# Performance work log

Measured on AMD Instinct MI355X. Metric: run time of the kernel, lower is better.

Reference implementation:

```python
import jax, jax.numpy as jnp
import numpy as np

COST_CLASS, COST_BBOX, COST_GIOU = 1.0, 5.0, 2.0
NUM_CLASSES = 80
BS, T, Q = 16, 32, 1024


def box_cxcywh_to_xyxy(b):
    cx, cy, w, h = jnp.split(b, 4, axis=-1)
    return jnp.concatenate([cx - 0.5 * w, cy - 0.5 * h, cx + 0.5 * w, cy + 0.5 * h], axis=-1)


def generalized_box_iou(b1, b2):
    # b1: [..., Q, 4] xyxy, b2: [..., 1, 4] xyxy -> [..., Q]
    area1 = (b1[..., 2] - b1[..., 0]) * (b1[..., 3] - b1[..., 1])
    area2 = (b2[..., 2] - b2[..., 0]) * (b2[..., 3] - b2[..., 1])
    lt = jnp.maximum(b1[..., :2], b2[..., :2])
    rb = jnp.minimum(b1[..., 2:], b2[..., 2:])
    wh = jnp.clip(rb - lt, 0.0)
    inter = wh[..., 0] * wh[..., 1]
    union = area1 + area2 - inter
    iou = inter / union
    lt_c = jnp.minimum(b1[..., :2], b2[..., :2])
    rb_c = jnp.maximum(b1[..., 2:], b2[..., 2:])
    wh_c = jnp.clip(rb_c - lt_c, 0.0)
    area_c = wh_c[..., 0] * wh_c[..., 1]
    return iou - (area_c - union) / area_c


def setup_inputs() -> dict:
    key = jax.random.key(0)
    k1, k2, k3, k4, k5 = jax.random.split(key, 5)
    return {
        "pred_logits": jax.random.normal(k1, (BS, T, Q, NUM_CLASSES), dtype=jnp.float32),
        "pred_logits_b": jax.random.normal(k2, (BS, T, Q, 2), dtype=jnp.float32),
        "pred_boxes": jax.random.uniform(k3, (BS, T, Q, 4), dtype=jnp.float32),
        "tgt_bbox": jax.random.uniform(k4, (BS, T, 1, 4), dtype=jnp.float32),
        "tgt_ids": jax.random.randint(k5, (BS * T,), 0, NUM_CLASSES, dtype=jnp.int64),
    }


def reference(pred_logits, pred_logits_b, pred_boxes, tgt_bbox, tgt_ids):
    bs, t, q = pred_logits.shape[0], pred_logits.shape[1], pred_logits.shape[2]
    # L1 cdist between each prediction and the single target box per frame: [bs,t,Q,1]
    cost_bbox = jnp.sum(jnp.abs(pred_boxes - tgt_bbox), axis=-1, keepdims=True)
    # GIoU cost: [bs,t,Q,1]
    cost_giou = -generalized_box_iou(
        box_cxcywh_to_xyxy(pred_boxes), box_cxcywh_to_xyxy(tgt_bbox)
    )[..., None]
    # binary objectness cost: -P(object): [bs,t,Q,1]
    cost_class = -jax.nn.softmax(pred_logits_b, axis=-1)[..., 1:2]
    C = COST_BBOX * cost_bbox + COST_CLASS * cost_class + COST_GIOU * cost_giou
    # Hungarian assignment on a Qx1 cost matrix == argmin over queries per frame
    rows = jnp.argmin(C[..., 0], axis=-1).reshape(bs * t)  # [bs*t] selected query idx
    # majority vote over all frames (the module returns the mode as the final idx)
    mode_idx = jnp.argmax(jnp.bincount(rows, length=q))
    return C, rows, mode_idx


if __name__ == "__main__":
    out = reference(**setup_inputs())
    print(out[0].shape, out[1].shape, out[2])
```

## Files before the change

kernel.cpp:

```cpp
#include <hip/hip_runtime.h>

#define NFRAMES 512
#define NQ      1024
#define CSIZE   (NFRAMES * NQ)

__global__ __launch_bounds__(256) void cost_argmin_kernel(
    const float* __restrict__ logits_b,
    const float* __restrict__ boxes,
    const float* __restrict__ tgt,
    float* __restrict__ out)
{
#pragma clang fp contract(off)
    const int f   = blockIdx.x;
    const int tid = threadIdx.x;

    const float4 tb = *reinterpret_cast<const float4*>(tgt + (size_t)f * 4);
    const float tx0 = tb.x - 0.5f * tb.z, ty0 = tb.y - 0.5f * tb.w;
    const float tx1 = tb.x + 0.5f * tb.z, ty1 = tb.y + 0.5f * tb.w;
    const float area2 = (tx1 - tx0) * (ty1 - ty0);

    const float* fb = boxes    + (size_t)f * NQ * 4;
    const float* fl = logits_b + (size_t)f * NQ * 2;
    float*       fc = out      + (size_t)f * NQ;

    float bestv = INFINITY;
    int   besti = 0;

    #pragma unroll
    for (int k = 0; k < 4; ++k) {
        const int q = tid + k * 256;
        const float4 pb = *reinterpret_cast<const float4*>(fb + q * 4);
        const float2 lg = *reinterpret_cast<const float2*>(fl + q * 2);

        const float cb = fabsf(pb.x - tb.x) + fabsf(pb.y - tb.y)
                       + fabsf(pb.z - tb.z) + fabsf(pb.w - tb.w);

        const float px0 = pb.x - 0.5f * pb.z, py0 = pb.y - 0.5f * pb.w;
        const float px1 = pb.x + 0.5f * pb.z, py1 = pb.y + 0.5f * pb.w;
        const float area1 = (px1 - px0) * (py1 - py0);

        const float ltx = fmaxf(px0, tx0), lty = fmaxf(py0, ty0);
        const float rbx = fminf(px1, tx1), rby = fminf(py1, ty1);
        const float whx = fmaxf(rbx - ltx, 0.0f), why = fmaxf(rby - lty, 0.0f);
        const float inter = whx * why;
        const float uni   = area1 + area2 - inter;
        const float iou   = inter / uni;

        const float lcx = fminf(px0, tx0), lcy = fminf(py0, ty0);
        const float rcx = fmaxf(px1, tx1), rcy = fmaxf(py1, ty1);
        const float wcx = fmaxf(rcx - lcx, 0.0f), wcy = fmaxf(rcy - lcy, 0.0f);
        const float areac = wcx * wcy;
        const float giou  = iou - (areac - uni) / areac;
        const float cg    = -giou;

        const float m  = fmaxf(lg.x, lg.y);
        const float e0 = expf(lg.x - m), e1 = expf(lg.y - m);
        const float cc = -(e1 / (e0 + e1));

        const float c = 5.0f * cb + 1.0f * cc + 2.0f * cg;
        fc[q] = c;

        if (c < bestv) { bestv = c; besti = q; }
    }

    __shared__ float sv[256];
    __shared__ int   si[256];
    sv[tid] = bestv; si[tid] = besti;
    __syncthreads();
    for (int s = 128; s > 0; s >>= 1) {
        if (tid < s) {
            const float v2 = sv[tid + s];
            const int   i2 = si[tid + s];
            if (v2 < sv[tid] || (v2 == sv[tid] && i2 < si[tid])) { sv[tid] = v2; si[tid] = i2; }
        }
        __syncthreads();
    }
    if (tid == 0) out[CSIZE + f] = (float)si[0];
}

__global__ __launch_bounds__(1024) void mode_kernel(float* __restrict__ out)
{
    __shared__ int counts[NQ];
    __shared__ int sc[NQ];
    __shared__ int si[NQ];
    const int tid = threadIdx.x;

    counts[tid] = 0;
    __syncthreads();
    if (tid < NFRAMES) {
        const int r = (int)out[CSIZE + tid];
        atomicAdd(&counts[r], 1);
    }
    __syncthreads();

    sc[tid] = counts[tid];
    si[tid] = tid;
    __syncthreads();
    for (int s = 512; s > 0; s >>= 1) {
        if (tid < s) {
            const int c2 = sc[tid + s];
            const int i2 = si[tid + s];
            if (c2 > sc[tid] || (c2 == sc[tid] && i2 < si[tid])) { sc[tid] = c2; si[tid] = i2; }
        }
        __syncthreads();
    }
    if (tid == 0) out[CSIZE + NFRAMES] = (float)si[0];
}

extern "C" void kernel_launch(void* const* d_in, const int* in_sizes, int n_in,
                              void* d_out, int out_size, void* d_ws, size_t ws_size,
                              hipStream_t stream) {
    const float* logits_b = (const float*)d_in[1];
    const float* boxes    = (const float*)d_in[2];
    const float* tgt      = (const float*)d_in[3];
    float* out = (float*)d_out;

    hipLaunchKernelGGL(cost_argmin_kernel, dim3(NFRAMES), dim3(256), 0, stream,
                       logits_b, boxes, tgt, out);
    hipLaunchKernelGGL(mode_kernel, dim3(1), dim3(1024), 0, stream, out);
}
```

Before: 210.0 us.

## Fuse mode computation into cost kernel via global histogram and last-block reduction

Removes the separate single-block mode kernel. Each block atomically adds its argmin row to a global histogram, and the last block to finish (found through an atomic counter) reduces the histogram to pick the mode. This saves one kernel launch and its serial dependency. In exchange it adds a hipMemsetAsync of the workspace on every call and global atomics with a thread fence.

```diff
diff --git a/kernel.cpp b/kernel.cpp
--- a/kernel.cpp
+++ b/kernel.cpp
@@ -4,15 +4,22 @@
 #define NQ      1024
 #define CSIZE   (NFRAMES * NQ)
 
-__global__ __launch_bounds__(256) void cost_argmin_kernel(
+__global__ __launch_bounds__(256) void fused_matcher_kernel(
     const float* __restrict__ logits_b,
     const float* __restrict__ boxes,
     const float* __restrict__ tgt,
-    float* __restrict__ out)
+    float* __restrict__ out,
+    int* __restrict__ bins,
+    int* __restrict__ counter)
 {
 #pragma clang fp contract(off)
     const int f   = blockIdx.x;
     const int tid = threadIdx.x;
+
+    __shared__ float sv[256];
+    __shared__ int   si[256];
+    __shared__ int   scc[256];
+    __shared__ int   is_last;
 
     const float4 tb = *reinterpret_cast<const float4*>(tgt + (size_t)f * 4);
     const float tx0 = tb.x - 0.5f * tb.z, ty0 = tb.y - 0.5f * tb.w;
@@ -63,8 +70,6 @@
         if (c < bestv) { bestv = c; besti = q; }
     }
 
-    __shared__ float sv[256];
-    __shared__ int   si[256];
     sv[tid] = bestv; si[tid] = besti;
     __syncthreads();
     for (int s = 128; s > 0; s >>= 1) {
@@ -75,36 +80,41 @@
         }
         __syncthreads();
     }
-    if (tid == 0) out[CSIZE + f] = (float)si[0];
-}
 
-__global__ __launch_bounds__(1024) void mode_kernel(float* __restrict__ out)
-{
-    __shared__ int counts[NQ];
-    __shared__ int sc[NQ];
-    __shared__ int si[NQ];
-    const int tid = threadIdx.x;
-
-    counts[tid] = 0;
-    __syncthreads();
-    if (tid < NFRAMES) {
-        const int r = (int)out[CSIZE + tid];
-        atomicAdd(&counts[r], 1);
+    if (tid == 0) {
+        const int row = si[0];
+        out[CSIZE + f] = (float)row;
+        atomicAdd(&bins[row], 1);
+        __threadfence();
+        const int old = __hip_atomic_fetch_add(counter, 1, __ATOMIC_ACQ_REL,
+                                               __HIP_MEMORY_SCOPE_AGENT);
+        is_last = (old == NFRAMES - 1) ? 1 : 0;
     }
     __syncthreads();
 
-    sc[tid] = counts[tid];
-    si[tid] = tid;
-    __syncthreads();
-    for (int s = 512; s > 0; s >>= 1) {
-        if (tid < s) {
-            const int c2 = sc[tid + s];
-            const int i2 = si[tid + s];
-            if (c2 > sc[tid] || (c2 == sc[tid] && i2 < si[tid])) { sc[tid] = c2; si[tid] = i2; }
+    if (is_last) {
+        int bc = -1, bi = 0;
+        #pragma unroll
+        for (int k = 0; k < 4; ++k) {
+            const int i = tid * 4 + k;
+            const int c = __hip_atomic_load(&bins[i], __ATOMIC_RELAXED,
+                                            __HIP_MEMORY_SCOPE_AGENT);
+            if (c > bc) { bc = c; bi = i; }
         }
+        scc[tid] = bc; si[tid] = bi;
         __syncthreads();
+        for (int s = 128; s > 0; s >>= 1) {
+            if (tid < s) {
+                const int c2 = scc[tid + s];
+                const int i2 = si[tid + s];
+                if (c2 > scc[tid] || (c2 == scc[tid] && i2 < si[tid])) {
+                    scc[tid] = c2; si[tid] = i2;
+                }
+            }
+            __syncthreads();
+        }
+        if (tid == 0) out[CSIZE + NFRAMES] = (float)si[0];
     }
-    if (tid == 0) out[CSIZE + NFRAMES] = (float)si[0];
 }
 
 extern "C" void kernel_launch(void* const* d_in, const int* in_sizes, int n_in,
@@ -113,9 +123,12 @@
     const float* logits_b = (const float*)d_in[1];
     const float* boxes    = (const float*)d_in[2];
     const float* tgt      = (const float*)d_in[3];
-    float* out = (float*)d_out;
+    float* out   = (float*)d_out;
+    int*   bins  = (int*)d_ws;
+    int*   cnt   = bins + NQ;
 
-    hipLaunchKernelGGL(cost_argmin_kernel, dim3(NFRAMES), dim3(256), 0, stream,
-                       logits_b, boxes, tgt, out);
-    hipLaunchKernelGGL(mode_kernel, dim3(1), dim3(1024), 0, stream, out);
+    hipMemsetAsync(d_ws, 0, (NQ + 1) * sizeof(int), stream);
+
+    hipLaunchKernelGGL(fused_matcher_kernel, dim3(NFRAMES), dim3(256), 0, stream,
+                       logits_b, boxes, tgt, out, bins, cnt);
 }
```

New measurement: 227.2 us. 1.08x slower.
